# Kernel tuning notes

Hardware: AMD Instinct MI355X
Metric: run time of the kernel (lower is better)

The kernel has to match this reference:

```python
import jax, jax.numpy as jnp
import numpy as np


def _bn(x, g, b):
    # per-feature batch norm over (batch, seq), training-style statistics
    mu = jnp.mean(x, axis=(0, 1), keepdims=True)
    var = jnp.var(x, axis=(0, 1), keepdims=True)
    return (x - mu) * jax.lax.rsqrt(var + 1e-5) * g + b


def _heads(x, H):
    B, S, D = x.shape
    return x.reshape(B, S, H, D // H).transpose(0, 2, 1, 3)  # [B,H,S,hd]


def _merge(x):
    B, H, S, hd = x.shape
    return x.transpose(0, 2, 1, 3).reshape(B, S, H * hd)


def _pos_encoding(S, D, dtype):
    p = jnp.arange(S, dtype=jnp.float32)[:, None]
    i = jnp.arange(D // 2, dtype=jnp.float32)[None, :]
    ang = p / jnp.power(10000.0, 2.0 * i / D)
    # interleave sin (even dims) and cos (odd dims)
    return jnp.stack([jnp.sin(ang), jnp.cos(ang)], axis=-1).reshape(S, D).astype(dtype)


def _forward(x, encod, embed, Wq, bq, Wk, bk, Wv, bv, g1, b1,
             Wq2, bq2, Wk2, bk2, Wv2, bv2, Wo2, bo2, g2, b2, Wf, bf,
             num_heads, N):
    D = embed.shape[1]
    emb = embed[x]                      # [B,S,D]
    S = emb.shape[1]
    # forward does embed + (embed + pos) == 2*embed + pos
    input_multi = 2.0 * emb + _pos_encoding(S, D, emb.dtype)
    scale1 = 1.0 / np.sqrt(D)           # original scales by sqrt(embed_dim)
    scale2 = 1.0 / np.sqrt(D // num_heads)
    for _ in range(N):
        q, k, v = jnp.split(input_multi, 3, axis=-1)   # each [B,S,D/3]
        Q = _heads(jax.nn.relu(q @ Wq + bq), num_heads)
        K = _heads(jax.nn.relu(k @ Wk + bk), num_heads)
        Vm = _heads(jax.nn.relu(v @ Wv + bv), num_heads)
        A = jax.nn.softmax(jnp.einsum('bhqd,bhkd->bhqk', Q, K) * scale1, axis=-1)
        sa = _merge(jnp.einsum('bhqk,bhkd->bhqd', A, Vm))
        t = _bn(input_multi + sa, g1, b1)
        # cross attention: q,k from encoder halves, v from decoder state
        eq, ek = jnp.split(encod, 2, axis=-1)          # each [B,S,D/2]
        Q2 = _heads(eq @ Wq2 + bq2, num_heads)
        K2 = _heads(ek @ Wk2 + bk2, num_heads)
        V2 = _heads(t @ Wv2 + bv2, num_heads)
        A2 = jax.nn.softmax(jnp.einsum('bhqd,bhkd->bhqk', Q2, K2) * scale2, axis=-1)
        m2 = _merge(jnp.einsum('bhqk,bhkd->bhqd', A2, V2)) @ Wo2 + bo2
        t = _bn(m2 + t, g2, b2)
        # add_norm_2 reused for the FFN residual, as in the source
        input_multi = _bn(t + (t @ Wf + bf), g2, b2)
    return input_multi


def setup_inputs() -> dict:
    B, S, D, H, V, N = 4, 1024, 768, 12, 32000, 2
    ks = jax.random.split(jax.random.key(0), 12)
    w = lambda k, shape: jax.random.normal(k, shape, jnp.float32) * 0.02
    zeros = lambda: jnp.zeros((D,), jnp.float32)
    ones = lambda: jnp.ones((D,), jnp.float32)
    return {
        'x': jax.random.randint(ks[0], (B, S), 0, V),
        'encod': jax.random.normal(ks[1], (B, S, D), jnp.float32),
        'embed': w(ks[2], (V, D)),
        'Wq': w(ks[3], (D // 3, D)), 'bq': zeros(),
        'Wk': w(ks[4], (D // 3, D)), 'bk': zeros(),
        'Wv': w(ks[5], (D // 3, D)), 'bv': zeros(),
        'g1': ones(), 'b1': zeros(),
        'Wq2': w(ks[6], (D // 2, D)), 'bq2': zeros(),
        'Wk2': w(ks[7], (D // 2, D)), 'bk2': zeros(),
        'Wv2': w(ks[8], (D, D)), 'bv2': zeros(),
        'Wo2': w(ks[9], (D, D)), 'bo2': zeros(),
        'g2': ones(), 'b2': zeros(),
        'Wf': w(ks[10], (D, D)), 'bf': zeros(),
        'num_heads': H, 'N': N,
    }


def reference(x, encod, embed, Wq, bq, Wk, bk, Wv, bv, g1, b1,
              Wq2, bq2, Wk2, bk2, Wv2, bv2, Wo2, bo2, g2, b2, Wf, bf,
              num_heads, N):
    return _forward(x, encod, embed, Wq, bq, Wk, bk, Wv, bv, g1, b1,
                    Wq2, bq2, Wk2, bk2, Wv2, bv2, Wo2, bo2, g2, b2, Wf, bf,
                    num_heads, N)
```

## Files before the change

kernel.cpp:

```cpp
#include <hip/hip_runtime.h>
#include <hip/hip_bf16.h>

#define B 4
#define S 1024
#define D 768
#define H 12
#define HD 64
#define MROWS (B * S)
#define NELEM (B * S * D)

typedef __attribute__((ext_vector_type(8))) short short8;
typedef __attribute__((ext_vector_type(4))) short s16x4;
typedef __attribute__((ext_vector_type(4))) float f32x4;

#define MFMA16(a, b, c) __builtin_amdgcn_mfma_f32_16x16x32_bf16(a, b, c, 0, 0, 0)

#define SWZ64(row, col)  ((col) ^ (((row) & 7) << 3))
#define SWZ32(row, col)  ((col) ^ ((((row) >> 1) & 3) << 3))
#define SWZ128(row, col) ((col) ^ (((row) & 15) << 3))

static __device__ __forceinline__ float bs2f(short s) {
    unsigned int u = ((unsigned int)(unsigned short)s) << 16;
    float f;
    __builtin_memcpy(&f, &u, 4);
    return f;
}
static __device__ __forceinline__ short f2bs(float f) {
    __hip_bfloat16 h = __float2bfloat16(f);
    return __builtin_bit_cast(short, h);
}
static __device__ __forceinline__ float loadin(const void* p, size_t i, int isb) {
    return isb ? bs2f(((const short*)p)[i]) : ((const float*)p)[i];
}

__global__ void detect_k(const void* p, int* flag) {
    const short* hb = (const short*)p;
    int t = threadIdx.x;
    int ins = 0;
    #pragma unroll
    for (int j = 0; j < 4; j++) {
        float v = bs2f(hb[(t * 4 + j) * 2]);
        if (!(v == v) || fabsf(v) > 1e3f || (v != 0.0f && fabsf(v) < 1e-20f)) ins++;
    }
    #pragma unroll
    for (int off = 32; off; off >>= 1) ins += __shfl_xor(ins, off);
    if (t == 0) *flag = (ins > 64) ? 0 : 1;
}

__global__ __launch_bounds__(256) void embed_pos_k(const int* __restrict__ x,
                                                   const void* __restrict__ embed,
                                                   float* __restrict__ outf,
                                                   short* __restrict__ outb,
                                                   const int* __restrict__ flg) {
    const int f = *flg;
    int bs = blockIdx.x;
    int tok = x[bs];
    int s = bs & (S - 1);
    for (int j = threadIdx.x; j < D; j += 256) {
        float e = loadin(embed, (size_t)tok * D + j, f);
        int i = j >> 1;
        float ang = (float)s * __expf(-9.210340371976184f * (2.0f * (float)i) / (float)D);
        float p = (j & 1) ? cosf(ang) : sinf(ang);
        float v = 2.0f * e + p;
        outf[bs * D + j] = v;
        outb[bs * D + j] = f2bs(v);
    }
}

struct WSegs {
    const void* src[8];
    short* dst[8];
    int K[8];
    const void* esrc;
    short* edst;
    float* statz;
};

__global__ __launch_bounds__(256) void prep_k(WSegs sg, const int* __restrict__ flg) {
    const int f = *flg;
    const int seg = blockIdx.z;
    const int t = threadIdx.x;
    if (seg == 8) {
        int tid = (blockIdx.y * 12 + blockIdx.x) * 256 + t;
        if (tid < 9216) sg.statz[tid] = 0.f;
        for (int i = tid; i < NELEM; i += 12 * 12 * 256)
            sg.edst[i] = f2bs(loadin(sg.esrc, i, f));
        return;
    }
    const int K = sg.K[seg];
    const int k0 = blockIdx.y * 64;
    if (k0 >= K) return;
    const void* src = sg.src[seg];
    short* dst = sg.dst[seg];
    __shared__ __align__(16) short Ts[64 * 72];
    int n0 = blockIdx.x * 64;
    int r = t >> 2, c4 = (t & 3) * 16;
    #pragma unroll
    for (int j = 0; j < 16; j++)
        Ts[r * 72 + c4 + j] = f2bs(loadin(src, (size_t)(k0 + r) * D + n0 + c4 + j, f));
    __syncthreads();
    int n = t >> 2, kc = (t & 3) * 16;
    short tmp[16];
    #pragma unroll
    for (int j = 0; j < 16; j++) tmp[j] = Ts[(kc + j) * 72 + n];
    short* dchunk = dst + (size_t)(n0 + n) * K + k0 + kc;
    *(short8*)&dchunk[0] = *(const short8*)&tmp[0];
    *(short8*)&dchunk[8] = *(const short8*)&tmp[8];
}

__global__ __launch_bounds__(256) void store_norm_k(const float* __restrict__ a,
                                                    const float* __restrict__ sums,
                                                    const void* __restrict__ g,
                                                    const void* __restrict__ beta,
                                                    void* __restrict__ out,
                                                    const int* __restrict__ flg) {
    const int f = *flg;
    int i = blockIdx.x * 256 + threadIdx.x;
    if (i < NELEM) {
        int ft = i % D;
        float mean = sums[ft] * (1.0f / (float)MROWS);
        float var = sums[D + ft] * (1.0f / (float)MROWS) - mean * mean;
        float sc = rsqrtf(var + 1e-5f) * loadin(g, ft, f);
        float y = (a[i] - mean) * sc + loadin(beta, ft, f);
        if (f) ((short*)out)[i] = f2bs(y);
        else   ((float*)out)[i] = y;
    }
}

struct GJob {
    const void* A;
    const short* WT;
    const void* bias;
    void* out;
    const float* resid;
    const float* bnsums;
    const void* bng;
    const void* bnb;
    float* sacc;
    int K;
    int aoff;
    int relu;
    int mode;
    int anorm;
    int rnorm;
};
struct GJobs { GJob j[3]; };

__global__ __launch_bounds__(256) void mgemm_k(GJobs js, const int* __restrict__ flg) {
    const GJob J = js.j[blockIdx.z];
    const int f = *flg;
    __shared__ __align__(16) short sb[64 * 72];
    __shared__ float ssb0[768];
    __shared__ float ssb1[768];
    short* As = sb;
    short* Bs = sb + 2048;
    const int t = threadIdx.x;
    const int wave = t >> 6, lane = t & 63;
    const int quad = lane >> 4, l16 = lane & 15;
    if (J.anorm) {
        for (int i = t; i < D; i += 256) {
            float mean = J.bnsums[i] * (1.0f / (float)MROWS);
            float var = J.bnsums[D + i] * (1.0f / (float)MROWS) - mean * mean;
            float sc = rsqrtf(var + 1e-5f) * loadin(J.bng, i, f);
            ssb0[i] = sc;
            ssb1[i] = loadin(J.bnb, i, f) - mean * sc;
        }
        __syncthreads();
    }
    int lin = blockIdx.y * gridDim.x + blockIdx.x;
    int per = (gridDim.x * gridDim.y) >> 3;
    int nl = (lin & 7) * per + (lin >> 3);
    const int n0 = (nl % gridDim.x) * 64;
    const int m0 = (nl / gridDim.x) * 64;
    const int wm = (wave >> 1) * 32;
    const int wn = (wave & 1) * 32;
    f32x4 acc[2][2];
    #pragma unroll
    for (int i = 0; i < 2; i++)
        #pragma unroll
        for (int j = 0; j < 2; j++) acc[i][j] = f32x4{0.f, 0.f, 0.f, 0.f};

    const int ar = t >> 2;
    const int ac = (t & 3) * 8;
    const int acs = SWZ32(ar, ac);
    const int K = J.K;
    for (int k0 = 0; k0 < K; k0 += 32) {
        if (J.anorm) {
            int ft = J.aoff + k0 + ac;
            const float* Af = (const float*)J.A + (size_t)(m0 + ar) * 768 + ft;
            f32x4 v0 = *(const f32x4*)&Af[0];
            f32x4 v1 = *(const f32x4*)&Af[4];
            f32x4 sc0 = *(const f32x4*)&ssb0[ft];
            f32x4 sc1 = *(const f32x4*)&ssb0[ft + 4];
            f32x4 sh0 = *(const f32x4*)&ssb1[ft];
            f32x4 sh1 = *(const f32x4*)&ssb1[ft + 4];
            short8 pk;
            #pragma unroll
            for (int e = 0; e < 4; e++) {
                pk[e]     = f2bs(v0[e] * sc0[e] + sh0[e]);
                pk[4 + e] = f2bs(v1[e] * sc1[e] + sh1[e]);
            }
            *(short8*)&As[ar * 32 + acs] = pk;
        } else {
            *(short8*)&As[ar * 32 + acs] =
                *(const short8*)&((const short*)J.A)[(size_t)(m0 + ar) * 768 + k0 + ac];
        }
        *(short8*)&Bs[ar * 32 + SWZ32(ar, ac)] =
            *(const short8*)&J.WT[(size_t)(n0 + ar) * K + k0 + ac];
        __syncthreads();
        short8 af[2], bfr[2];
        #pragma unroll
        for (int i = 0; i < 2; i++) {
            int arow = wm + i * 16 + l16;
            af[i] = *(const short8*)&As[arow * 32 + SWZ32(arow, quad * 8)];
        }
        #pragma unroll
        for (int j = 0; j < 2; j++) {
            int brow = wn + j * 16 + l16;
            bfr[j] = *(const short8*)&Bs[brow * 32 + SWZ32(brow, quad * 8)];
        }
        #pragma unroll
        for (int i = 0; i < 2; i++)
            #pragma unroll
            for (int j = 0; j < 2; j++)
                acc[i][j] = MFMA16(af[i], bfr[j], acc[i][j]);
        __syncthreads();
    }
    if (J.mode == 3) {
        #pragma unroll
        for (int j = 0; j < 2; j++) {
            int coll = wn + j * 16 + l16;
            float bv = loadin(J.bias, n0 + coll, f);
            #pragma unroll
            for (int i = 0; i < 2; i++) {
                int rowl = wm + i * 16 + quad * 4;
                s16x4 pk;
                #pragma unroll
                for (int r = 0; r < 4; r++) {
                    float v = acc[i][j][r] + bv;
                    if (J.relu) v = fmaxf(v, 0.f);
                    pk[r] = f2bs(v);
                }
                *(s16x4*)&sb[coll * 72 + rowl] = pk;
            }
        }
        __syncthreads();
        int hd = t >> 2, c = (t & 3) * 16;
        int b = m0 >> 10, s0 = m0 & (S - 1), h = n0 >> 6;
        short* dst = (short*)J.out + (((size_t)(b * H + h) * HD + hd) * S + s0 + c);
        *(short8*)&dst[0] = *(const short8*)&sb[hd * 72 + c];
        *(short8*)&dst[8] = *(const short8*)&sb[hd * 72 + c + 8];
    } else {
        #pragma unroll
        for (int j = 0; j < 2; j++) {
            int col = n0 + wn + j * 16 + l16;
            float bv = loadin(J.bias, col, f);
            float rsc = 1.f, rsh = 0.f;
            if (J.rnorm) {
                float mean = J.bnsums[col] * (1.0f / (float)MROWS);
                float var = J.bnsums[D + col] * (1.0f / (float)MROWS) - mean * mean;
                rsc = rsqrtf(var + 1e-5f) * loadin(J.bng, col, f);
                rsh = loadin(J.bnb, col, f) - mean * rsc;
            }
            float s1 = 0.f, s2 = 0.f;
            #pragma unroll
            for (int i = 0; i < 2; i++) {
                int rowb = m0 + wm + i * 16 + quad * 4;
                #pragma unroll
                for (int r = 0; r < 4; r++) {
                    float v = acc[i][j][r] + bv;
                    if (J.relu) v = fmaxf(v, 0.f);
                    int row = rowb + r;
                    if (J.mode == 2) {
                        size_t idx = (size_t)row * D + col;
                        if (J.resid) {
                            float rv = J.resid[idx];
                            v += J.rnorm ? (rv * rsc + rsh) : rv;
                        }
                        ((float*)J.out)[idx] = v;
                        s1 += v;
                        s2 += v * v;
                    } else if (J.mode == 1) {
                        size_t idx = (((size_t)(row >> 10) * H + (col >> 6)) * S + (row & (S - 1))) * HD + (col & 63);
                        ((short*)J.out)[idx] = f2bs(v);
                    } else {
                        ((short*)J.out)[(size_t)row * D + col] = f2bs(v);
                    }
                }
            }
            if (J.mode == 2 && J.sacc) {
                s1 += __shfl_xor(s1, 16); s1 += __shfl_xor(s1, 32);
                s2 += __shfl_xor(s2, 16); s2 += __shfl_xor(s2, 32);
                if (quad == 0) {
                    atomicAdd(&J.sacc[col], s1);
                    atomicAdd(&J.sacc[D + col], s2);
                }
            }
        }
    }
}

__global__ __launch_bounds__(256) void mfma_attn_fo_k(const short* __restrict__ Q,
                                                      const short* __restrict__ Km,
                                                      const short* __restrict__ Vt,
                                                      void* __restrict__ out,
                                                      const float* __restrict__ resid,
                                                      const float* __restrict__ rsums,
                                                      const void* __restrict__ rg,
                                                      const void* __restrict__ rb,
                                                      float* __restrict__ sacc,
                                                      float scale, int obf,
                                                      const int* __restrict__ flg) {
    __shared__ __align__(16) short Ks[128 * 64];
    __shared__ __align__(16) short Vs[64 * 128];
    __shared__ __align__(16) short Ps[4][16 * 136];
    const int fl = *flg;
    const int qt = blockIdx.y;
    const int bh = blockIdx.x;
    const int b = bh / H, h = bh % H;
    const int t = threadIdx.x;
    const int wave = t >> 6, lane = t & 63, quad = lane >> 4, l16 = lane & 15;
    const float sc2 = scale * 1.44269504089f;
    const short* Qh = Q + (size_t)bh * S * HD;
    const short* Kh = Km + (size_t)bh * S * HD;
    const short* Vh = Vt + (size_t)bh * S * HD;
    const int qrow = qt * 64 + wave * 16 + l16;
    short8 qf0 = *(const short8*)&Qh[(size_t)qrow * 64 + quad * 8];
    short8 qf1 = *(const short8*)&Qh[(size_t)qrow * 64 + 32 + quad * 8];
    short8 ones;
    #pragma unroll
    for (int j = 0; j < 8; j++) ones[j] = (short)0x3F80;
    f32x4 o[4];
    f32x4 ls = f32x4{0.f, 0.f, 0.f, 0.f};
    float m_i[4];
    #pragma unroll
    for (int nt = 0; nt < 4; nt++) o[nt] = f32x4{0.f, 0.f, 0.f, 0.f};
    #pragma unroll
    for (int r = 0; r < 4; r++) m_i[r] = -1e30f;
    const int krow = t >> 1, kc0 = (t & 1) * 32;
    const int vhd = t >> 2, vkc = (t & 3) * 32;
    const short* kbase = &Kh[(size_t)krow * 64 + kc0];
    const short* vbase = &Vh[(size_t)vhd * S + vkc];

    short8 kreg[4], vreg[4];
    #pragma unroll
    for (int j = 0; j < 4; j++) kreg[j] = *(const short8*)&kbase[j * 8];
    #pragma unroll
    for (int j = 0; j < 4; j++) vreg[j] = *(const short8*)&vbase[j * 8];
    #pragma unroll
    for (int j = 0; j < 4; j++)
        *(short8*)&Ks[krow * 64 + SWZ64(krow, kc0 + j * 8)] = kreg[j];
    #pragma unroll
    for (int j = 0; j < 4; j++)
        *(short8*)&Vs[vhd * 128 + SWZ128(vhd, vkc + j * 8)] = vreg[j];
    __syncthreads();

    for (int kt = 0; kt < S; kt += 128) {
        if (kt + 128 < S) {
            #pragma unroll
            for (int j = 0; j < 4; j++)
                kreg[j] = *(const short8*)&kbase[(size_t)(kt + 128) * 64 + j * 8];
            #pragma unroll
            for (int j = 0; j < 4; j++)
                vreg[j] = *(const short8*)&vbase[kt + 128 + j * 8];
        }
        f32x4 sf[8];
        #pragma unroll
        for (int nt = 0; nt < 8; nt++) {
            int kr = nt * 16 + l16;
            short8 kb0 = *(const short8*)&Ks[kr * 64 + SWZ64(kr, quad * 8)];
            short8 kb1 = *(const short8*)&Ks[kr * 64 + SWZ64(kr, 32 + quad * 8)];
            f32x4 c = f32x4{0.f, 0.f, 0.f, 0.f};
            c = MFMA16(qf0, kb0, c);
            c = MFMA16(qf1, kb1, c);
            sf[nt] = c;
        }
        float mx[4];
        #pragma unroll
        for (int r = 0; r < 4; r++) {
            float m = sf[0][r];
            #pragma unroll
            for (int nt = 1; nt < 8; nt++) m = fmaxf(m, sf[nt][r]);
            m = fmaxf(m, __shfl_xor(m, 1));
            m = fmaxf(m, __shfl_xor(m, 2));
            m = fmaxf(m, __shfl_xor(m, 4));
            m = fmaxf(m, __shfl_xor(m, 8));
            mx[r] = m;
        }
        bool need = false;
        #pragma unroll
        for (int r = 0; r < 4; r++) need |= ((mx[r] - m_i[r]) * sc2 > 8.0f);
        if (__any(need)) {
            #pragma unroll
            for (int r = 0; r < 4; r++) {
                float mnew = fmaxf(m_i[r], mx[r]);
                float alpha = exp2f((m_i[r] - mnew) * sc2);
                m_i[r] = mnew;
                ls[r] *= alpha;
                #pragma unroll
                for (int nt = 0; nt < 4; nt++) o[nt][r] *= alpha;
            }
        }
        #pragma unroll
        for (int nt = 0; nt < 8; nt++)
            #pragma unroll
            for (int r = 0; r < 4; r++)
                Ps[wave][(quad * 4 + r) * 136 + nt * 16 + l16] =
                    f2bs(exp2f((sf[nt][r] - m_i[r]) * sc2));
        short8 pa[4];
        #pragma unroll
        for (int kc = 0; kc < 4; kc++)
            pa[kc] = *(const short8*)&Ps[wave][l16 * 136 + kc * 32 + quad * 8];
        #pragma unroll
        for (int nt = 0; nt < 4; nt++) {
            int vr = nt * 16 + l16;
            #pragma unroll
            for (int kc = 0; kc < 4; kc++) {
                short8 vb = *(const short8*)&Vs[vr * 128 + SWZ128(vr, kc * 32 + quad * 8)];
                o[nt] = MFMA16(pa[kc], vb, o[nt]);
            }
        }
        #pragma unroll
        for (int kc = 0; kc < 4; kc++) ls = MFMA16(pa[kc], ones, ls);
        __syncthreads();
        if (kt + 128 < S) {
            #pragma unroll
            for (int j = 0; j < 4; j++)
                *(short8*)&Ks[krow * 64 + SWZ64(krow, kc0 + j * 8)] = kreg[j];
            #pragma unroll
            for (int j = 0; j < 4; j++)
                *(short8*)&Vs[vhd * 128 + SWZ128(vhd, vkc + j * 8)] = vreg[j];
        }
        __syncthreads();
    }
    float inv[4];
    #pragma unroll
    for (int r = 0; r < 4; r++) inv[r] = 1.0f / ls[r];
    #pragma unroll
    for (int nt = 0; nt < 4; nt++) {
        int col = h * HD + nt * 16 + l16;
        float rsc = 1.f, rsh = 0.f;
        if (rsums) {
            float mean = rsums[col] * (1.0f / (float)MROWS);
            float var = rsums[D + col] * (1.0f / (float)MROWS) - mean * mean;
            rsc = rsqrtf(var + 1e-5f) * loadin(rg, col, fl);
            rsh = loadin(rb, col, fl) - mean * rsc;
        }
        float s1 = 0.f, s2 = 0.f;
        #pragma unroll
        for (int r = 0; r < 4; r++) {
            int row = b * S + qt * 64 + wave * 16 + quad * 4 + r;
            size_t idx = (size_t)row * D + col;
            float v = o[nt][r] * inv[r];
            if (obf) {
                ((short*)out)[idx] = f2bs(v);
            } else {
                if (resid) {
                    float rv = resid[idx];
                    v += rsums ? (rv * rsc + rsh) : rv;
                }
                ((float*)out)[idx] = v;
                s1 += v;
                s2 += v * v;
            }
        }
        if (sacc) {
            s1 += __shfl_xor(s1, 16); s1 += __shfl_xor(s1, 32);
            s2 += __shfl_xor(s2, 16); s2 += __shfl_xor(s2, 32);
            if (quad == 0) {
                atomicAdd(&sacc[col], s1);
                atomicAdd(&sacc[D + col], s2);
            }
        }
    }
}

extern "C" void kernel_launch(void* const* d_in, const int* in_sizes, int n_in,
                              void* d_out, int out_size, void* d_ws, size_t ws_size,
                              hipStream_t stream) {
    const int* x = (const int*)d_in[0];
    const short* encod = (const short*)d_in[1];
    const short* embed = (const short*)d_in[2];
    const short* Wq = (const short*)d_in[3];
    const short* bq = (const short*)d_in[4];
    const short* Wk = (const short*)d_in[5];
    const short* bk = (const short*)d_in[6];
    const short* Wv = (const short*)d_in[7];
    const short* bv = (const short*)d_in[8];
    const short* g1 = (const short*)d_in[9];
    const short* b1 = (const short*)d_in[10];
    const short* Wq2 = (const short*)d_in[11];
    const short* bq2 = (const short*)d_in[12];
    const short* Wk2 = (const short*)d_in[13];
    const short* bk2 = (const short*)d_in[14];
    const short* Wv2 = (const short*)d_in[15];
    const short* bv2 = (const short*)d_in[16];
    const short* Wo2 = (const short*)d_in[17];
    const short* bo2 = (const short*)d_in[18];
    const short* g2 = (const short*)d_in[19];
    const short* b2 = (const short*)d_in[20];
    const short* Wf = (const short*)d_in[21];
    const short* bf_ = (const short*)d_in[22];

    short* HBase = (short*)d_ws;
    #define HB(i) (HBase + (size_t)(i) * NELEM)
    float* IMf = (float*)HB(0);
    short* IMb = HB(2);
    short* Q2h = HB(3);
    short* K2h = HB(4);
    short* WTp = HB(5);
    short* WTq  = WTp;
    short* WTk  = WTp + 196608;
    short* WTv  = WTp + 393216;
    short* WTq2 = WTp + 589824;
    short* WTk2 = WTp + 884736;
    short* WTv2 = WTp + 1179648;
    short* WTo2 = WTp + 1769472;
    short* WTf  = WTp + 2359296;
    short* Qbh = HB(6);
    short* Kbh = HB(7);
    short* Vth = HB(9);
    float* T1f = (float*)HB(10);
    float* Ff  = (float*)HB(12);
    short* A2b = HB(15);
    float* T2f = (float*)HB(16);
    short* Eb  = Qbh;
    float* SU = (float*)HB(18);
    #define SUMS(it, bn) (SU + (size_t)((it) * 3 + (bn)) * 2 * D)
    int*   flg  = (int*)(SU + 12 * D);

    const dim3 gGrid(12, 64);
    const dim3 aGrid(B * H, S / 64);
    const int EB = (NELEM + 255) / 256;
    const float scale1 = 0.03608439182435161f;
    const float scale2 = 0.125f;

    detect_k<<<1, 64, 0, stream>>>(encod, flg);
    embed_pos_k<<<MROWS, 256, 0, stream>>>(x, embed, IMf, IMb, flg);

    WSegs sg;
    sg.src[0] = Wq;  sg.dst[0] = WTq;  sg.K[0] = 256;
    sg.src[1] = Wk;  sg.dst[1] = WTk;  sg.K[1] = 256;
    sg.src[2] = Wv;  sg.dst[2] = WTv;  sg.K[2] = 256;
    sg.src[3] = Wq2; sg.dst[3] = WTq2; sg.K[3] = 384;
    sg.src[4] = Wk2; sg.dst[4] = WTk2; sg.K[4] = 384;
    sg.src[5] = Wv2; sg.dst[5] = WTv2; sg.K[5] = 768;
    sg.src[6] = Wo2; sg.dst[6] = WTo2; sg.K[6] = 768;
    sg.src[7] = Wf;  sg.dst[7] = WTf;  sg.K[7] = 768;
    sg.esrc = encod; sg.edst = Eb; sg.statz = SU;
    prep_k<<<dim3(12, 12, 9), 256, 0, stream>>>(sg, flg);

    {
        GJobs js;
        js.j[0] = GJob{Eb,       WTq2, bq2, Q2h, nullptr, nullptr, nullptr, nullptr, nullptr, 384, 0, 0, 1, 0, 0};
        js.j[1] = GJob{Eb + 384, WTk2, bk2, K2h, nullptr, nullptr, nullptr, nullptr, nullptr, 384, 0, 0, 1, 0, 0};
        js.j[2] = js.j[0];
        mgemm_k<<<dim3(12, 64, 2), 256, 0, stream>>>(js, flg);
    }

    for (int it = 0; it < 2; it++) {
        {
            GJobs js;
            if (it == 0) {
                js.j[0] = GJob{IMb,       WTq, bq, Qbh, nullptr, nullptr, nullptr, nullptr, nullptr, 256, 0,   1, 1, 0, 0};
                js.j[1] = GJob{IMb + 256, WTk, bk, Kbh, nullptr, nullptr, nullptr, nullptr, nullptr, 256, 0,   1, 1, 0, 0};
                js.j[2] = GJob{IMb + 512, WTv, bv, Vth, nullptr, nullptr, nullptr, nullptr, nullptr, 256, 0,   1, 3, 0, 0};
            } else {
                js.j[0] = GJob{Ff, WTq, bq, Qbh, nullptr, SUMS(0, 2), g2, b2, nullptr, 256, 0,   1, 1, 1, 0};
                js.j[1] = GJob{Ff, WTk, bk, Kbh, nullptr, SUMS(0, 2), g2, b2, nullptr, 256, 256, 1, 1, 1, 0};
                js.j[2] = GJob{Ff, WTv, bv, Vth, nullptr, SUMS(0, 2), g2, b2, nullptr, 256, 512, 1, 3, 1, 0};
            }
            mgemm_k<<<dim3(12, 64, 3), 256, 0, stream>>>(js, flg);
        }
        if (it == 0)
            mfma_attn_fo_k<<<aGrid, 256, 0, stream>>>(Qbh, Kbh, Vth, T1f, IMf,
                    nullptr, nullptr, nullptr, SUMS(0, 0), scale1, 0, flg);
        else
            mfma_attn_fo_k<<<aGrid, 256, 0, stream>>>(Qbh, Kbh, Vth, T1f, Ff,
                    SUMS(0, 2), g2, b2, SUMS(1, 0), scale1, 0, flg);
        {
            GJobs js;
            js.j[0] = GJob{T1f, WTv2, bv2, Vth, nullptr, SUMS(it, 0), g1, b1, nullptr, 768, 0, 0, 3, 1, 0};
            js.j[1] = js.j[0]; js.j[2] = js.j[0];
            mgemm_k<<<gGrid, 256, 0, stream>>>(js, flg);
        }
        mfma_attn_fo_k<<<aGrid, 256, 0, stream>>>(Q2h, K2h, Vth, A2b, nullptr,
                nullptr, nullptr, nullptr, nullptr, scale2, 1, flg);
        {
            GJobs js;
            js.j[0] = GJob{A2b, WTo2, bo2, T2f, T1f, SUMS(it, 0), g1, b1, SUMS(it, 1), 768, 0, 0, 2, 0, 1};
            js.j[1] = js.j[0]; js.j[2] = js.j[0];
            mgemm_k<<<gGrid, 256, 0, stream>>>(js, flg);
        }
        {
            GJobs js;
            js.j[0] = GJob{T2f, WTf, bf_, Ff, T2f, SUMS(it, 1), g2, b2, SUMS(it, 2), 768, 0, 0, 2, 1, 1};
            js.j[1] = js.j[0]; js.j[2] = js.j[0];
            mgemm_k<<<gGrid, 256, 0, stream>>>(js, flg);
        }
    }

    store_norm_k<<<EB, 256, 0, stream>>>(Ff, SUMS(1, 2), g2, b2, d_out, flg);
}
```

Baseline: 618.9 us.

## Double-buffer GEMM K-tiles at 64 depth and read attention K/V directly from global

The GEMM kernel now stages 64-wide K tiles into two LDS buffers and prefetches the next tile into registers while computing the current one. This halves the loop trip count and drops one barrier per iteration. The attention kernel no longer stages K and V through shared memory: each wave loads its MFMA fragments straight from global memory and all block barriers are removed. The aim is to cut synchronisation and LDS traffic, at the cost of redundant global/L2 reads of K and V across the four waves. The mode-3 epilogue's scratch buffer is moved onto the A tile buffer.

```diff
diff --git a/kernel.cpp b/kernel.cpp
--- a/kernel.cpp
+++ b/kernel.cpp
@@ -16,8 +16,6 @@
 #define MFMA16(a, b, c) __builtin_amdgcn_mfma_f32_16x16x32_bf16(a, b, c, 0, 0, 0)
 
 #define SWZ64(row, col)  ((col) ^ (((row) & 7) << 3))
-#define SWZ32(row, col)  ((col) ^ ((((row) >> 1) & 3) << 3))
-#define SWZ128(row, col) ((col) ^ (((row) & 15) << 3))
 
 static __device__ __forceinline__ float bs2f(short s) {
     unsigned int u = ((unsigned int)(unsigned short)s) << 16;
@@ -149,11 +147,10 @@
 __global__ __launch_bounds__(256) void mgemm_k(GJobs js, const int* __restrict__ flg) {
     const GJob J = js.j[blockIdx.z];
     const int f = *flg;
-    __shared__ __align__(16) short sb[64 * 72];
+    __shared__ __align__(16) short As[2][64 * 64];
+    __shared__ __align__(16) short Bs[2][64 * 64];
     __shared__ float ssb0[768];
     __shared__ float ssb1[768];
-    short* As = sb;
-    short* Bs = sb + 2048;
     const int t = threadIdx.x;
     const int wave = t >> 6, lane = t & 63;
     const int quad = lane >> 4, l16 = lane & 15;
@@ -181,52 +178,95 @@
         for (int j = 0; j < 2; j++) acc[i][j] = f32x4{0.f, 0.f, 0.f, 0.f};
 
     const int ar = t >> 2;
-    const int ac = (t & 3) * 8;
-    const int acs = SWZ32(ar, ac);
+    const int ac = (t & 3) * 16;
+    const int wsz0 = SWZ64(ar, ac);
+    const int wsz1 = SWZ64(ar, ac + 8);
     const int K = J.K;
-    for (int k0 = 0; k0 < K; k0 += 32) {
+
+    auto stageA = [&](int k0, short8& r0, short8& r1) {
         if (J.anorm) {
             int ft = J.aoff + k0 + ac;
             const float* Af = (const float*)J.A + (size_t)(m0 + ar) * 768 + ft;
             f32x4 v0 = *(const f32x4*)&Af[0];
             f32x4 v1 = *(const f32x4*)&Af[4];
-            f32x4 sc0 = *(const f32x4*)&ssb0[ft];
-            f32x4 sc1 = *(const f32x4*)&ssb0[ft + 4];
-            f32x4 sh0 = *(const f32x4*)&ssb1[ft];
-            f32x4 sh1 = *(const f32x4*)&ssb1[ft + 4];
-            short8 pk;
+            f32x4 v2 = *(const f32x4*)&Af[8];
+            f32x4 v3 = *(const f32x4*)&Af[12];
+            f32x4 c0 = *(const f32x4*)&ssb0[ft];
+            f32x4 c1 = *(const f32x4*)&ssb0[ft + 4];
+            f32x4 c2 = *(const f32x4*)&ssb0[ft + 8];
+            f32x4 c3 = *(const f32x4*)&ssb0[ft + 12];
+            f32x4 h0 = *(const f32x4*)&ssb1[ft];
+            f32x4 h1 = *(const f32x4*)&ssb1[ft + 4];
+            f32x4 h2 = *(const f32x4*)&ssb1[ft + 8];
+            f32x4 h3 = *(const f32x4*)&ssb1[ft + 12];
             #pragma unroll
             for (int e = 0; e < 4; e++) {
-                pk[e]     = f2bs(v0[e] * sc0[e] + sh0[e]);
-                pk[4 + e] = f2bs(v1[e] * sc1[e] + sh1[e]);
-            }
-            *(short8*)&As[ar * 32 + acs] = pk;
+                r0[e]     = f2bs(v0[e] * c0[e] + h0[e]);
+                r0[4 + e] = f2bs(v1[e] * c1[e] + h1[e]);
+                r1[e]     = f2bs(v2[e] * c2[e] + h2[e]);
+                r1[4 + e] = f2bs(v3[e] * c3[e] + h3[e]);
+            }
         } else {
-            *(short8*)&As[ar * 32 + acs] =
-                *(const short8*)&((const short*)J.A)[(size_t)(m0 + ar) * 768 + k0 + ac];
-        }
-        *(short8*)&Bs[ar * 32 + SWZ32(ar, ac)] =
-            *(const short8*)&J.WT[(size_t)(n0 + ar) * K + k0 + ac];
+            const short* Ab = (const short*)J.A + (size_t)(m0 + ar) * 768 + k0 + ac;
+            r0 = *(const short8*)&Ab[0];
+            r1 = *(const short8*)&Ab[8];
+        }
+    };
+
+    {
+        short8 a0, a1, b0, b1;
+        stageA(0, a0, a1);
+        const short* Wb = &J.WT[(size_t)(n0 + ar) * K + ac];
+        b0 = *(const short8*)&Wb[0];
+        b1 = *(const short8*)&Wb[8];
+        *(short8*)&As[0][ar * 64 + wsz0] = a0;
+        *(short8*)&As[0][ar * 64 + wsz1] = a1;
+        *(short8*)&Bs[0][ar * 64 + wsz0] = b0;
+        *(short8*)&Bs[0][ar * 64 + wsz1] = b1;
+    }
+    __syncthreads();
+
+    int cur = 0;
+    for (int k0 = 0; k0 < K; k0 += 64) {
+        short8 na0, na1, nb0, nb1;
+        const bool more = (k0 + 64 < K);
+        if (more) {
+            stageA(k0 + 64, na0, na1);
+            const short* Wb = &J.WT[(size_t)(n0 + ar) * K + k0 + 64 + ac];
+            nb0 = *(const short8*)&Wb[0];
+            nb1 = *(const short8*)&Wb[8];
+        }
+        #pragma unroll
+        for (int kk = 0; kk < 2; kk++) {
+            short8 af[2], bfr[2];
+            #pragma unroll
+            for (int i = 0; i < 2; i++) {
+                int arow = wm + i * 16 + l16;
+                af[i] = *(const short8*)&As[cur][arow * 64 + SWZ64(arow, kk * 32 + quad * 8)];
+            }
+            #pragma unroll
+            for (int j = 0; j < 2; j++) {
+                int brow = wn + j * 16 + l16;
+                bfr[j] = *(const short8*)&Bs[cur][brow * 64 + SWZ64(brow, kk * 32 + quad * 8)];
+            }
+            #pragma unroll
+            for (int i = 0; i < 2; i++)
+                #pragma unroll
+                for (int j = 0; j < 2; j++)
+                    acc[i][j] = MFMA16(af[i], bfr[j], acc[i][j]);
+        }
+        if (more) {
+            *(short8*)&As[cur ^ 1][ar * 64 + wsz0] = na0;
+            *(short8*)&As[cur ^ 1][ar * 64 + wsz1] = na1;
+            *(short8*)&Bs[cur ^ 1][ar * 64 + wsz0] = nb0;
+            *(short8*)&Bs[cur ^ 1][ar * 64 + wsz1] = nb1;
+        }
         __syncthreads();
-        short8 af[2], bfr[2];
-        #pragma unroll
-        for (int i = 0; i < 2; i++) {
-            int arow = wm + i * 16 + l16;
-            af[i] = *(const short8*)&As[arow * 32 + SWZ32(arow, quad * 8)];
-        }
-        #pragma unroll
-        for (int j = 0; j < 2; j++) {
-            int brow = wn + j * 16 + l16;
-            bfr[j] = *(const short8*)&Bs[brow * 32 + SWZ32(brow, quad * 8)];
-        }
-        #pragma unroll
-        for (int i = 0; i < 2; i++)
-            #pragma unroll
-            for (int j = 0; j < 2; j++)
-                acc[i][j] = MFMA16(af[i], bfr[j], acc[i][j]);
-        __syncthreads();
-    }
+        cur ^= 1;
+    }
+
     if (J.mode == 3) {
+        short* sb = &As[0][0];
         #pragma unroll
         for (int j = 0; j < 2; j++) {
             int coll = wn + j * 16 + l16;
@@ -311,8 +351,6 @@
                                                       float* __restrict__ sacc,
                                                       float scale, int obf,
                                                       const int* __restrict__ flg) {
-    __shared__ __align__(16) short Ks[128 * 64];
-    __shared__ __align__(16) short Vs[64 * 128];
     __shared__ __align__(16) short Ps[4][16 * 136];
     const int fl = *flg;
     const int qt = blockIdx.y;
@@ -337,39 +375,14 @@
     for (int nt = 0; nt < 4; nt++) o[nt] = f32x4{0.f, 0.f, 0.f, 0.f};
     #pragma unroll
     for (int r = 0; r < 4; r++) m_i[r] = -1e30f;
-    const int krow = t >> 1, kc0 = (t & 1) * 32;
-    const int vhd = t >> 2, vkc = (t & 3) * 32;
-    const short* kbase = &Kh[(size_t)krow * 64 + kc0];
-    const short* vbase = &Vh[(size_t)vhd * S + vkc];
-
-    short8 kreg[4], vreg[4];
-    #pragma unroll
-    for (int j = 0; j < 4; j++) kreg[j] = *(const short8*)&kbase[j * 8];
-    #pragma unroll
-    for (int j = 0; j < 4; j++) vreg[j] = *(const short8*)&vbase[j * 8];
-    #pragma unroll
-    for (int j = 0; j < 4; j++)
-        *(short8*)&Ks[krow * 64 + SWZ64(krow, kc0 + j * 8)] = kreg[j];
-    #pragma unroll
-    for (int j = 0; j < 4; j++)
-        *(short8*)&Vs[vhd * 128 + SWZ128(vhd, vkc + j * 8)] = vreg[j];
-    __syncthreads();
 
     for (int kt = 0; kt < S; kt += 128) {
-        if (kt + 128 < S) {
-            #pragma unroll
-            for (int j = 0; j < 4; j++)
-                kreg[j] = *(const short8*)&kbase[(size_t)(kt + 128) * 64 + j * 8];
-            #pragma unroll
-            for (int j = 0; j < 4; j++)
-                vreg[j] = *(const short8*)&vbase[kt + 128 + j * 8];
-        }
         f32x4 sf[8];
         #pragma unroll
         for (int nt = 0; nt < 8; nt++) {
-            int kr = nt * 16 + l16;
-            short8 kb0 = *(const short8*)&Ks[kr * 64 + SWZ64(kr, quad * 8)];
-            short8 kb1 = *(const short8*)&Ks[kr * 64 + SWZ64(kr, 32 + quad * 8)];
+            const short* kp = &Kh[(size_t)(kt + nt * 16 + l16) * 64 + quad * 8];
+            short8 kb0 = *(const short8*)&kp[0];
+            short8 kb1 = *(const short8*)&kp[32];
             f32x4 c = f32x4{0.f, 0.f, 0.f, 0.f};
             c = MFMA16(qf0, kb0, c);
             c = MFMA16(qf1, kb1, c);
@@ -413,25 +426,15 @@
             pa[kc] = *(const short8*)&Ps[wave][l16 * 136 + kc * 32 + quad * 8];
         #pragma unroll
         for (int nt = 0; nt < 4; nt++) {
-            int vr = nt * 16 + l16;
+            const short* vp = &Vh[(size_t)(nt * 16 + l16) * S + kt + quad * 8];
             #pragma unroll
             for (int kc = 0; kc < 4; kc++) {
-                short8 vb = *(const short8*)&Vs[vr * 128 + SWZ128(vr, kc * 32 + quad * 8)];
+                short8 vb = *(const short8*)&vp[kc * 32];
                 o[nt] = MFMA16(pa[kc], vb, o[nt]);
             }
         }
         #pragma unroll
         for (int kc = 0; kc < 4; kc++) ls = MFMA16(pa[kc], ones, ls);
-        __syncthreads();
-        if (kt + 128 < S) {
-            #pragma unroll
-            for (int j = 0; j < 4; j++)
-                *(short8*)&Ks[krow * 64 + SWZ64(krow, kc0 + j * 8)] = kreg[j];
-            #pragma unroll
-            for (int j = 0; j < 4; j++)
-                *(short8*)&Vs[vhd * 128 + SWZ128(vhd, vkc + j * 8)] = vreg[j];
-        }
-        __syncthreads();
     }
     float inv[4];
     #pragma unroll
```

Measured after the change: 796.3 us. 28.7% more time.
